# Kernel tuning notes

Measured on AMD Instinct MI355X. Metric: run time of the kernel, lower is better.

## Reference

```python
import jax, jax.numpy as jnp
import numpy as np

E = 64  # embedding_size
N_NODES = 100000
N_FACTS = 100000  # ground facts per relation
ARITY_GROUPS = {1: 2, 2: 3, 3: 2, 4: 1}  # arity -> number of relations with that arity


def mish(x):
    return x * jnp.tanh(jax.nn.softplus(x))


def _group_messages(node_embeddings, idx, wi, bi, wo, bo, arity):
    # idx: [G, F*arity] flat node indices for G relations of this arity
    G, L = idx.shape
    x = node_embeddings[idx]                      # [G, F*arity, E] gather
    x = x.reshape(G, L // arity, arity * E)       # [G, F, arity*E]
    h = mish(jnp.einsum('gfi,goi->gfo', x, wi) + bi[:, None, :])
    y = jnp.einsum('gfi,goi->gfo', h, wo) + bo[:, None, :]
    msgs = (x + y).reshape(-1, E)                 # residual, back to [G*F*arity, E]
    return msgs, idx.reshape(-1)


def setup_inputs():
    key = jax.random.key(0)
    ks = jax.random.split(key, 16)
    inp = {"node_embeddings": jax.random.normal(ks[0], (N_NODES, E), jnp.float32)}
    k = 1
    for a, G in ARITY_GROUPS.items():
        d = a * E
        inp[f"idx_a{a}"] = jax.random.randint(ks[k], (G, N_FACTS * a), 0, N_NODES); k += 1
        inp[f"wi_a{a}"] = jax.random.normal(ks[k], (G, d, d), jnp.float32) / np.sqrt(d).astype(np.float32); k += 1
        inp[f"bi_a{a}"] = jnp.zeros((G, d), jnp.float32)
        inp[f"wo_a{a}"] = jax.random.normal(ks[k], (G, d, d), jnp.float32) / np.sqrt(d).astype(np.float32); k += 1
        inp[f"bo_a{a}"] = jnp.zeros((G, d), jnp.float32)
    return inp


def reference(node_embeddings,
              idx_a1, wi_a1, bi_a1, wo_a1, bo_a1,
              idx_a2, wi_a2, bi_a2, wo_a2, bo_a2,
              idx_a3, wi_a3, bi_a3, wo_a3, bo_a3,
              idx_a4, wi_a4, bi_a4, wo_a4, bo_a4):
    groups = [
        (idx_a1, wi_a1, bi_a1, wo_a1, bo_a1, 1),
        (idx_a2, wi_a2, bi_a2, wo_a2, bo_a2, 2),
        (idx_a3, wi_a3, bi_a3, wo_a3, bo_a3, 3),
        (idx_a4, wi_a4, bi_a4, wo_a4, bo_a4, 4),
    ]
    msgs_list, idx_list = [], []
    for idx, wi, bi, wo, bo, a in groups:  # fixed small loop over arity groups
        m, i = _group_messages(node_embeddings, idx, wi, bi, wo, bo, a)
        msgs_list.append(m)
        idx_list.append(i)
    output_messages = jnp.concatenate(msgs_list, axis=0)   # [sum G*F*a, E]
    output_indices = jnp.concatenate(idx_list, axis=0)
    return output_messages, output_indices
```

## Files before the change

kernel.cpp:

```cpp
#include <hip/hip_runtime.h>
#include <hip/hip_bf16.h>

#define NF 100000
#define TM 64
#define NB 1563

typedef __attribute__((ext_vector_type(8))) short bf16x8;
typedef __attribute__((ext_vector_type(4))) short bf16x4;
typedef __attribute__((ext_vector_type(4))) float f32x4;

__device__ __forceinline__ short bfs(float x) {
    union { __hip_bfloat16 h; short s; } u;
    u.h = __float2bfloat16(x);
    return u.s;
}

__device__ __forceinline__ float b2f(short s) {
    union { float f; unsigned u; } u;
    u.u = ((unsigned)(unsigned short)s) << 16;
    return u.f;
}

__device__ __forceinline__ bf16x8 cvt8(const float4 a, const float4 b) {
    bf16x8 r;
    r[0] = bfs(a.x); r[1] = bfs(a.y); r[2] = bfs(a.z); r[3] = bfs(a.w);
    r[4] = bfs(b.x); r[5] = bfs(b.y); r[6] = bfs(b.z); r[7] = bfs(b.w);
    return r;
}

__device__ __forceinline__ float mish_f(float v) {
    float t = __expf(v);
    float p = t * (t + 2.0f);
    float r = v * p * __builtin_amdgcn_rcpf(p + 2.0f);
    return (v > 20.0f) ? v : r;
}

struct CvtA {
    const float* src[8];
    long pre[9];
    int  Dv[8];
    const float* emb;
    long embElems;
};

__global__ __launch_bounds__(256)
void cvt_all(CvtA a, __hip_bfloat16* __restrict__ dst) {
    long e = ((long)blockIdx.x * 256 + threadIdx.x) * 8;
    if (e < a.embElems) {
        const float4* s = (const float4*)(a.emb + e);
        *(bf16x8*)(dst + e) = cvt8(s[0], s[1]);
        return;
    }
    long we = e - a.embElems;
    if (we >= a.pre[8]) return;
    int j = 0;
    #pragma unroll
    for (int q = 0; q < 8; q++) if (we >= a.pre[q + 1]) j = q + 1;
    long le = we - a.pre[j];
    const int D = a.Dv[j];
    int g = (int)(le / ((long)D * D));
    int rem = (int)(le - (long)g * D * D);
    int n = rem / D;
    int k = rem - n * D;
    const float4* s = (const float4*)(a.src[j] + le);
    long off = a.embElems + a.pre[j] + (long)g * D * D + (long)(k >> 5) * 32 * D + n * 32 + (k & 31);
    *(bf16x8*)(dst + off) = cvt8(s[0], s[1]);
}

template<int D, int A, int MINW>
__global__ __launch_bounds__(256, MINW)
void msg3_kernel(const __hip_bfloat16* __restrict__ emb,
                 const int* __restrict__ idx,
                 const __hip_bfloat16* __restrict__ wi, const float* __restrict__ bi,
                 const __hip_bfloat16* __restrict__ wo, const float* __restrict__ bo,
                 float* __restrict__ out_msgs, float* __restrict__ out_idx)
{
    constexpr int DP = D + 8;
    constexpr int CT = D / 64;
    constexpr int KS = D / 32;
    constexpr int RC = D / 8;
    constexpr int CH = (TM * RC) / 256;
    constexpr bool FULLW = (D <= 128);
    __shared__ __hip_bfloat16 buf[TM][DP];

    const int g    = blockIdx.y;
    const int f0   = blockIdx.x * TM;
    const int tid  = threadIdx.x;
    const int lane = tid & 63;
    const int w    = tid >> 6;
    const long gFA = (long)g * NF * A;
    const int valid = min(TM, NF - f0);
    const int* idx_g = idx + gFA + (long)f0 * A;

    const int ar = lane & 15;
    const int kg = lane >> 4;
    const int c0 = w * (D / 4);
    const long wlane = (long)g * D * D + (long)(c0 + ar) * 32 + kg * 8;

    {
        int nodes[CH];
        #pragma unroll
        for (int j = 0; j < CH; j++) {
            int c = tid + j * 256;
            int r = c / RC;
            nodes[j] = (r < valid) ? idx_g[r * A + ((c % RC) >> 3)] : idx_g[0];
        }
        bf16x8 v[CH];
        #pragma unroll
        for (int j = 0; j < CH; j++) {
            int c = tid + j * 256;
            v[j] = *(const bf16x8*)(emb + (long)nodes[j] * 64 + (((c % RC) * 8) & 63));
        }
        #pragma unroll
        for (int j = 0; j < CH; j++) {
            int c = tid + j * 256;
            *(bf16x8*)(&buf[c / RC][(c % RC) * 8]) = v[j];
        }
        if (tid < valid * A)
            __builtin_nontemporal_store((float)idx_g[tid], &out_idx[gFA + (long)f0 * A + tid]);
    }

    f32x4 acc[4][CT];
    #pragma unroll
    for (int rt = 0; rt < 4; rt++)
        #pragma unroll
        for (int ct = 0; ct < CT; ct++) acc[rt][ct] = (f32x4)0.0f;

    if constexpr (FULLW) {
        bf16x8 wia[KS][CT];
        #pragma unroll
        for (int ks = 0; ks < KS; ks++)
            #pragma unroll
            for (int ct = 0; ct < CT; ct++)
                wia[ks][ct] = *(const bf16x8*)(wi + wlane + (long)ks * 32 * D + ct * 512);

        __syncthreads();

        #pragma unroll
        for (int ks = 0; ks < KS; ks++) {
            const int kk = ks * 32;
            bf16x8 xb[4];
            #pragma unroll
            for (int rt = 0; rt < 4; rt++) xb[rt] = *(const bf16x8*)(&buf[rt * 16 + ar][kk + kg * 8]);
            #pragma unroll
            for (int ct = 0; ct < CT; ct++)
                #pragma unroll
                for (int rt = 0; rt < 4; rt++)
                    acc[rt][ct] = __builtin_amdgcn_mfma_f32_16x16x32_bf16(wia[ks][ct], xb[rt], acc[rt][ct], 0, 0, 0);
        }

        bf16x8 woa[KS][CT];
        #pragma unroll
        for (int ks = 0; ks < KS; ks++)
            #pragma unroll
            for (int ct = 0; ct < CT; ct++)
                woa[ks][ct] = *(const bf16x8*)(wo + wlane + (long)ks * 32 * D + ct * 512);

        bf16x4 res[4][CT];
        #pragma unroll
        for (int ct = 0; ct < CT; ct++) {
            const int cb = c0 + ct * 16 + kg * 4;
            #pragma unroll
            for (int rt = 0; rt < 4; rt++)
                res[rt][ct] = *(const bf16x4*)(&buf[rt * 16 + ar][cb]);
        }
        __syncthreads();

        #pragma unroll
        for (int ct = 0; ct < CT; ct++) {
            const int cb = c0 + ct * 16 + kg * 4;
            const float4 bi4 = *(const float4*)(bi + g * D + cb);
            #pragma unroll
            for (int rt = 0; rt < 4; rt++) {
                bf16x4 hv;
                hv[0] = bfs(mish_f(acc[rt][ct][0] + bi4.x));
                hv[1] = bfs(mish_f(acc[rt][ct][1] + bi4.y));
                hv[2] = bfs(mish_f(acc[rt][ct][2] + bi4.z));
                hv[3] = bfs(mish_f(acc[rt][ct][3] + bi4.w));
                *(bf16x4*)(&buf[rt * 16 + ar][cb]) = hv;
            }
        }
        __syncthreads();

        #pragma unroll
        for (int rt = 0; rt < 4; rt++)
            #pragma unroll
            for (int ct = 0; ct < CT; ct++) acc[rt][ct] = (f32x4)0.0f;

        #pragma unroll
        for (int ks = 0; ks < KS; ks++) {
            const int kk = ks * 32;
            bf16x8 hb[4];
            #pragma unroll
            for (int rt = 0; rt < 4; rt++) hb[rt] = *(const bf16x8*)(&buf[rt * 16 + ar][kk + kg * 8]);
            #pragma unroll
            for (int ct = 0; ct < CT; ct++)
                #pragma unroll
                for (int rt = 0; rt < 4; rt++)
                    acc[rt][ct] = __builtin_amdgcn_mfma_f32_16x16x32_bf16(woa[ks][ct], hb[rt], acc[rt][ct], 0, 0, 0);
        }

        float* ob = out_msgs + (gFA + (long)f0 * A) * 64;
        #pragma unroll
        for (int ct = 0; ct < CT; ct++) {
            const int cb = c0 + ct * 16 + kg * 4;
            const float4 bo4 = *(const float4*)(bo + g * D + cb);
            #pragma unroll
            for (int rt = 0; rt < 4; rt++) {
                const int r = rt * 16 + ar;
                f32x4 o;
                o[0] = acc[rt][ct][0] + bo4.x + b2f(res[rt][ct][0]);
                o[1] = acc[rt][ct][1] + bo4.y + b2f(res[rt][ct][1]);
                o[2] = acc[rt][ct][2] + bo4.z + b2f(res[rt][ct][2]);
                o[3] = acc[rt][ct][3] + bo4.w + b2f(res[rt][ct][3]);
                if (r < valid)
                    __builtin_nontemporal_store(o, (f32x4*)(ob + (long)r * D + cb));
            }
        }
    } else {
        bf16x8 wcur[CT];
        #pragma unroll
        for (int ct = 0; ct < CT; ct++)
            wcur[ct] = *(const bf16x8*)(wi + wlane + ct * 512);

        __syncthreads();

        #pragma unroll
        for (int ks = 0; ks < KS; ks++) {
            bf16x8 wnx[CT];
            if (ks + 1 < KS)
                #pragma unroll
                for (int ct = 0; ct < CT; ct++)
                    wnx[ct] = *(const bf16x8*)(wi + wlane + (long)(ks + 1) * 32 * D + ct * 512);
            const int kk = ks * 32;
            bf16x8 xb[4];
            #pragma unroll
            for (int rt = 0; rt < 4; rt++) xb[rt] = *(const bf16x8*)(&buf[rt * 16 + ar][kk + kg * 8]);
            #pragma unroll
            for (int ct = 0; ct < CT; ct++)
                #pragma unroll
                for (int rt = 0; rt < 4; rt++)
                    acc[rt][ct] = __builtin_amdgcn_mfma_f32_16x16x32_bf16(wcur[ct], xb[rt], acc[rt][ct], 0, 0, 0);
            if (ks + 1 < KS)
                #pragma unroll
                for (int ct = 0; ct < CT; ct++) wcur[ct] = wnx[ct];
        }

        #pragma unroll
        for (int ct = 0; ct < CT; ct++)
            wcur[ct] = *(const bf16x8*)(wo + wlane + ct * 512);

        bf16x4 res[4][CT];
        #pragma unroll
        for (int ct = 0; ct < CT; ct++) {
            const int cb = c0 + ct * 16 + kg * 4;
            #pragma unroll
            for (int rt = 0; rt < 4; rt++)
                res[rt][ct] = *(const bf16x4*)(&buf[rt * 16 + ar][cb]);
        }
        __syncthreads();

        #pragma unroll
        for (int ct = 0; ct < CT; ct++) {
            const int cb = c0 + ct * 16 + kg * 4;
            const float4 bi4 = *(const float4*)(bi + g * D + cb);
            #pragma unroll
            for (int rt = 0; rt < 4; rt++) {
                bf16x4 hv;
                hv[0] = bfs(mish_f(acc[rt][ct][0] + bi4.x));
                hv[1] = bfs(mish_f(acc[rt][ct][1] + bi4.y));
                hv[2] = bfs(mish_f(acc[rt][ct][2] + bi4.z));
                hv[3] = bfs(mish_f(acc[rt][ct][3] + bi4.w));
                *(bf16x4*)(&buf[rt * 16 + ar][cb]) = hv;
            }
        }
        __syncthreads();

        #pragma unroll
        for (int rt = 0; rt < 4; rt++)
            #pragma unroll
            for (int ct = 0; ct < CT; ct++) acc[rt][ct] = (f32x4)0.0f;

        #pragma unroll
        for (int ks = 0; ks < KS; ks++) {
            bf16x8 wnx[CT];
            if (ks + 1 < KS)
                #pragma unroll
                for (int ct = 0; ct < CT; ct++)
                    wnx[ct] = *(const bf16x8*)(wo + wlane + (long)(ks + 1) * 32 * D + ct * 512);
            const int kk = ks * 32;
            bf16x8 hb[4];
            #pragma unroll
            for (int rt = 0; rt < 4; rt++) hb[rt] = *(const bf16x8*)(&buf[rt * 16 + ar][kk + kg * 8]);
            #pragma unroll
            for (int ct = 0; ct < CT; ct++)
                #pragma unroll
                for (int rt = 0; rt < 4; rt++)
                    acc[rt][ct] = __builtin_amdgcn_mfma_f32_16x16x32_bf16(wcur[ct], hb[rt], acc[rt][ct], 0, 0, 0);
            if (ks + 1 < KS)
                #pragma unroll
                for (int ct = 0; ct < CT; ct++) wcur[ct] = wnx[ct];
        }

        float* ob = out_msgs + (gFA + (long)f0 * A) * 64;
        #pragma unroll
        for (int ct = 0; ct < CT; ct++) {
            const int cb = c0 + ct * 16 + kg * 4;
            const float4 bo4 = *(const float4*)(bo + g * D + cb);
            #pragma unroll
            for (int rt = 0; rt < 4; rt++) {
                const int r = rt * 16 + ar;
                f32x4 o;
                o[0] = acc[rt][ct][0] + bo4.x + b2f(res[rt][ct][0]);
                o[1] = acc[rt][ct][1] + bo4.y + b2f(res[rt][ct][1]);
                o[2] = acc[rt][ct][2] + bo4.z + b2f(res[rt][ct][2]);
                o[3] = acc[rt][ct][3] + bo4.w + b2f(res[rt][ct][3]);
                if (r < valid)
                    __builtin_nontemporal_store(o, (f32x4*)(ob + (long)r * D + cb));
            }
        }
    }
}

template<int D, int A, int MINW>
__global__ __launch_bounds__(256, MINW)
void msg_kernel(const float* __restrict__ embv,
                const int* __restrict__ idx,
                const float* __restrict__ wiv, const float* __restrict__ bi,
                const float* __restrict__ wov, const float* __restrict__ bo,
                float* __restrict__ out_msgs, float* __restrict__ out_idx)
{
    constexpr int DP = D + 8;
    constexpr int CT = D / 64;
    constexpr int KS = D / 32;
    constexpr int RC = D / 8;
    __shared__ __hip_bfloat16 buf[TM][DP];

    const int g    = blockIdx.y;
    const int f0   = blockIdx.x * TM;
    const int tid  = threadIdx.x;
    const int lane = tid & 63;
    const int w    = tid >> 6;
    const long gFA = (long)g * NF * A;
    const int valid = min(TM, NF - f0);

    {
        const int* idx_g = idx + gFA + (long)f0 * A;
        #pragma unroll
        for (int c = tid; c < TM * RC; c += 256) {
            int r = c / RC;
            int i = (c - r * RC) * 8;
            bf16x8 v = (bf16x8)0;
            if (r < valid) {
                int node = idx_g[r * A + (i >> 6)];
                const float4* s = (const float4*)(embv + (long)node * 64 + (i & 63));
                v = cvt8(s[0], s[1]);
            }
            *(bf16x8*)(&buf[r][i]) = v;
        }
        if (tid < valid * A) out_idx[gFA + (long)f0 * A + tid] = (float)idx_g[tid];
    }
    __syncthreads();

    const int ar = lane & 15;
    const int kg = lane >> 4;
    const int c0 = w * (D / 4);
    const long wbase = (long)g * D * D;

    f32x4 acc[4][CT];
    #pragma unroll
    for (int rt = 0; rt < 4; rt++)
        #pragma unroll
        for (int ct = 0; ct < CT; ct++) acc[rt][ct] = (f32x4)0.0f;

    #pragma unroll
    for (int ks = 0; ks < KS; ks++) {
        const int kk = ks * 32;
        bf16x8 xb[4];
        #pragma unroll
        for (int rt = 0; rt < 4; rt++) xb[rt] = *(const bf16x8*)(&buf[rt * 16 + ar][kk + kg * 8]);
        #pragma unroll
        for (int ct = 0; ct < CT; ct++) {
            const float4* bp = (const float4*)(wiv + wbase + (long)(c0 + ct * 16 + ar) * D + kk + kg * 8);
            bf16x8 wf = cvt8(bp[0], bp[1]);
            #pragma unroll
            for (int rt = 0; rt < 4; rt++)
                acc[rt][ct] = __builtin_amdgcn_mfma_f32_16x16x32_bf16(wf, xb[rt], acc[rt][ct], 0, 0, 0);
        }
    }

    bf16x4 res[4][CT];
    #pragma unroll
    for (int ct = 0; ct < CT; ct++) {
        const int cb = c0 + ct * 16 + kg * 4;
        #pragma unroll
        for (int rt = 0; rt < 4; rt++)
            res[rt][ct] = *(const bf16x4*)(&buf[rt * 16 + ar][cb]);
    }
    __syncthreads();

    #pragma unroll
    for (int ct = 0; ct < CT; ct++) {
        const int cb = c0 + ct * 16 + kg * 4;
        const float4 bi4 = *(const float4*)(bi + g * D + cb);
        #pragma unroll
        for (int rt = 0; rt < 4; rt++) {
            bf16x4 hv;
            hv[0] = bfs(mish_f(acc[rt][ct][0] + bi4.x));
            hv[1] = bfs(mish_f(acc[rt][ct][1] + bi4.y));
            hv[2] = bfs(mish_f(acc[rt][ct][2] + bi4.z));
            hv[3] = bfs(mish_f(acc[rt][ct][3] + bi4.w));
            *(bf16x4*)(&buf[rt * 16 + ar][cb]) = hv;
        }
    }
    __syncthreads();

    #pragma unroll
    for (int rt = 0; rt < 4; rt++)
        #pragma unroll
        for (int ct = 0; ct < CT; ct++) acc[rt][ct] = (f32x4)0.0f;

    #pragma unroll
    for (int ks = 0; ks < KS; ks++) {
        const int kk = ks * 32;
        bf16x8 hb[4];
        #pragma unroll
        for (int rt = 0; rt < 4; rt++) hb[rt] = *(const bf16x8*)(&buf[rt * 16 + ar][kk + kg * 8]);
        #pragma unroll
        for (int ct = 0; ct < CT; ct++) {
            const float4* bp = (const float4*)(wov + wbase + (long)(c0 + ct * 16 + ar) * D + kk + kg * 8);
            bf16x8 wf = cvt8(bp[0], bp[1]);
            #pragma unroll
            for (int rt = 0; rt < 4; rt++)
                acc[rt][ct] = __builtin_amdgcn_mfma_f32_16x16x32_bf16(wf, hb[rt], acc[rt][ct], 0, 0, 0);
        }
    }

    {
        float* ob = out_msgs + (gFA + (long)f0 * A) * 64;
        #pragma unroll
        for (int ct = 0; ct < CT; ct++) {
            const int cb = c0 + ct * 16 + kg * 4;
            const float4 bo4 = *(const float4*)(bo + g * D + cb);
            #pragma unroll
            for (int rt = 0; rt < 4; rt++) {
                const int r = rt * 16 + ar;
                float4 o;
                o.x = acc[rt][ct][0] + bo4.x + b2f(res[rt][ct][0]);
                o.y = acc[rt][ct][1] + bo4.y + b2f(res[rt][ct][1]);
                o.z = acc[rt][ct][2] + bo4.z + b2f(res[rt][ct][2]);
                o.w = acc[rt][ct][3] + bo4.w + b2f(res[rt][ct][3]);
                if (r < valid) *(float4*)(ob + (long)r * D + cb) = o;
            }
        }
    }
}

extern "C" void kernel_launch(void* const* d_in, const int* in_sizes, int n_in,
                              void* d_out, int out_size, void* d_ws, size_t ws_size,
                              hipStream_t stream) {
    const float* emb_f = (const float*)d_in[0];
    const int Gs[4] = {2, 3, 2, 1};
    const int Ds[4] = {64, 128, 192, 256};

    const int*   idx_a[4];
    const float *wi_f[4], *bi_f[4], *wo_f[4], *bo_f[4];
    for (int k = 0; k < 4; k++) {
        idx_a[k] = (const int*)d_in[1 + 5 * k];
        wi_f[k]  = (const float*)d_in[2 + 5 * k];
        bi_f[k]  = (const float*)d_in[3 + 5 * k];
        wo_f[k]  = (const float*)d_in[4 + 5 * k];
        bo_f[k]  = (const float*)d_in[5 + 5 * k];
    }

    float* out = (float*)d_out;
    const long MSG_ELEMS = 115200000L;
    const long rowOff[4] = {0, 200000, 800000, 1400000};
    float* om[4]; float* oi[4];
    for (int k = 0; k < 4; k++) {
        om[k] = out + rowOff[k] * 64;
        oi[k] = out + MSG_ELEMS + rowOff[k];
    }

    const long EMB_ELEMS = 6400000L;
    long wPre[9]; wPre[0] = 0;
    int  wD[8];
    for (int k = 0; k < 4; k++) {
        long we = (long)Gs[k] * Ds[k] * Ds[k];
        wPre[2 * k + 1] = wPre[2 * k] + we;
        wPre[2 * k + 2] = wPre[2 * k + 1] + we;
        wD[2 * k] = Ds[k]; wD[2 * k + 1] = Ds[k];
    }
    const long NEED = (EMB_ELEMS + wPre[8]) * 2;

    if (ws_size >= (size_t)NEED) {
        __hip_bfloat16* emb_b = (__hip_bfloat16*)d_ws;
        __hip_bfloat16* w_b   = emb_b + EMB_ELEMS;

        CvtA ca;
        for (int k = 0; k < 4; k++) { ca.src[2 * k] = wi_f[k]; ca.src[2 * k + 1] = wo_f[k]; }
        for (int j = 0; j < 9; j++) ca.pre[j] = wPre[j];
        for (int j = 0; j < 8; j++) ca.Dv[j] = wD[j];
        ca.emb = emb_f;
        ca.embElems = EMB_ELEMS;
        long totChunks = (EMB_ELEMS + wPre[8]) / 8;
        cvt_all<<<dim3((totChunks + 255) / 256), dim3(256), 0, stream>>>(ca, emb_b);

        const __hip_bfloat16 *wi_b[4], *wo_b[4];
        for (int k = 0; k < 4; k++) { wi_b[k] = w_b + wPre[2 * k]; wo_b[k] = w_b + wPre[2 * k + 1]; }

        msg3_kernel<64, 1, 4><<<dim3(NB, 2), 256, 0, stream>>>(
            emb_b, idx_a[0], wi_b[0], bi_f[0], wo_b[0], bo_f[0], om[0], oi[0]);
        msg3_kernel<128, 2, 4><<<dim3(NB, 3), 256, 0, stream>>>(
            emb_b, idx_a[1], wi_b[1], bi_f[1], wo_b[1], bo_f[1], om[1], oi[1]);
        msg3_kernel<192, 3, 4><<<dim3(NB, 2), 256, 0, stream>>>(
            emb_b, idx_a[2], wi_b[2], bi_f[2], wo_b[2], bo_f[2], om[2], oi[2]);
        msg3_kernel<256, 4, 3><<<dim3(NB, 1), 256, 0, stream>>>(
            emb_b, idx_a[3], wi_b[3], bi_f[3], wo_b[3], bo_f[3], om[3], oi[3]);
    } else {
        msg_kernel<64, 1, 4><<<dim3(NB, 2), 256, 0, stream>>>(
            emb_f, idx_a[0], wi_f[0], bi_f[0], wo_f[0], bo_f[0], om[0], oi[0]);
        msg_kernel<128, 2, 4><<<dim3(NB, 3), 256, 0, stream>>>(
            emb_f, idx_a[1], wi_f[1], bi_f[1], wo_f[1], bo_f[1], om[1], oi[1]);
        msg_kernel<192, 3, 4><<<dim3(NB, 2), 256, 0, stream>>>(
            emb_f, idx_a[2], wi_f[2], bi_f[2], wo_f[2], bo_f[2], om[2], oi[2]);
        msg_kernel<256, 4, 3><<<dim3(NB, 1), 256, 0, stream>>>(
            emb_f, idx_a[3], wi_f[3], bi_f[3], wo_f[3], bo_f[3], om[3], oi[3]);
    }
}
```

Before: 207.3 us.

## Fuse four arity kernels into one launch with per-block dispatch

Replaces the four per-arity kernel launches with a single fused kernel that picks the arity group from the block index, heaviest groups first, sharing one maximal LDS buffer. The intent is to remove launch gaps and tail effects between the per-arity kernels and let the groups overlap on the device. For D=256 a new mode streams weights from global memory per k-step without register double-buffering, and the large-D residual is re-gathered from the bf16 embeddings at store time instead of held in registers. This cuts register pressure but adds extra gather loads, and the shared LDS size and the single launch-bounds setting of 4 may reduce occupancy for the small-D blocks.

```diff
diff --git a/kernel.cpp b/kernel.cpp
--- a/kernel.cpp
+++ b/kernel.cpp
@@ -67,24 +67,22 @@
     *(bf16x8*)(dst + off) = cvt8(s[0], s[1]);
 }
 
-template<int D, int A, int MINW>
-__global__ __launch_bounds__(256, MINW)
-void msg3_kernel(const __hip_bfloat16* __restrict__ emb,
-                 const int* __restrict__ idx,
-                 const __hip_bfloat16* __restrict__ wi, const float* __restrict__ bi,
-                 const __hip_bfloat16* __restrict__ wo, const float* __restrict__ bo,
-                 float* __restrict__ out_msgs, float* __restrict__ out_idx)
+template<int D, int A, int WMODE>
+__device__ __forceinline__ void body(
+    int fb, int g,
+    const __hip_bfloat16* __restrict__ emb, const int* __restrict__ idx,
+    const __hip_bfloat16* __restrict__ wi, const float* __restrict__ bi,
+    const __hip_bfloat16* __restrict__ wo, const float* __restrict__ bo,
+    float* __restrict__ out_msgs, float* __restrict__ out_idx,
+    __hip_bfloat16* __restrict__ buf)
 {
     constexpr int DP = D + 8;
     constexpr int CT = D / 64;
     constexpr int KS = D / 32;
     constexpr int RC = D / 8;
     constexpr int CH = (TM * RC) / 256;
-    constexpr bool FULLW = (D <= 128);
-    __shared__ __hip_bfloat16 buf[TM][DP];
-
-    const int g    = blockIdx.y;
-    const int f0   = blockIdx.x * TM;
+
+    const int f0   = fb * TM;
     const int tid  = threadIdx.x;
     const int lane = tid & 63;
     const int w    = tid >> 6;
@@ -114,7 +112,7 @@
         #pragma unroll
         for (int j = 0; j < CH; j++) {
             int c = tid + j * 256;
-            *(bf16x8*)(&buf[c / RC][(c % RC) * 8]) = v[j];
+            *(bf16x8*)(buf + (c / RC) * DP + (c % RC) * 8) = v[j];
         }
         if (tid < valid * A)
             __builtin_nontemporal_store((float)idx_g[tid], &out_idx[gFA + (long)f0 * A + tid]);
@@ -126,7 +124,7 @@
         #pragma unroll
         for (int ct = 0; ct < CT; ct++) acc[rt][ct] = (f32x4)0.0f;
 
-    if constexpr (FULLW) {
+    if constexpr (WMODE == 0) {
         bf16x8 wia[KS][CT];
         #pragma unroll
         for (int ks = 0; ks < KS; ks++)
@@ -141,7 +139,8 @@
             const int kk = ks * 32;
             bf16x8 xb[4];
             #pragma unroll
-            for (int rt = 0; rt < 4; rt++) xb[rt] = *(const bf16x8*)(&buf[rt * 16 + ar][kk + kg * 8]);
+            for (int rt = 0; rt < 4; rt++)
+                xb[rt] = *(const bf16x8*)(buf + (rt * 16 + ar) * DP + kk + kg * 8);
             #pragma unroll
             for (int ct = 0; ct < CT; ct++)
                 #pragma unroll
@@ -162,7 +161,7 @@
             const int cb = c0 + ct * 16 + kg * 4;
             #pragma unroll
             for (int rt = 0; rt < 4; rt++)
-                res[rt][ct] = *(const bf16x4*)(&buf[rt * 16 + ar][cb]);
+                res[rt][ct] = *(const bf16x4*)(buf + (rt * 16 + ar) * DP + cb);
         }
         __syncthreads();
 
@@ -177,7 +176,7 @@
                 hv[1] = bfs(mish_f(acc[rt][ct][1] + bi4.y));
                 hv[2] = bfs(mish_f(acc[rt][ct][2] + bi4.z));
                 hv[3] = bfs(mish_f(acc[rt][ct][3] + bi4.w));
-                *(bf16x4*)(&buf[rt * 16 + ar][cb]) = hv;
+                *(bf16x4*)(buf + (rt * 16 + ar) * DP + cb) = hv;
             }
         }
         __syncthreads();
@@ -192,7 +191,8 @@
             const int kk = ks * 32;
             bf16x8 hb[4];
             #pragma unroll
-            for (int rt = 0; rt < 4; rt++) hb[rt] = *(const bf16x8*)(&buf[rt * 16 + ar][kk + kg * 8]);
+            for (int rt = 0; rt < 4; rt++)
+                hb[rt] = *(const bf16x8*)(buf + (rt * 16 + ar) * DP + kk + kg * 8);
             #pragma unroll
             for (int ct = 0; ct < CT; ct++)
                 #pragma unroll
@@ -219,45 +219,45 @@
         }
     } else {
         bf16x8 wcur[CT];
-        #pragma unroll
-        for (int ct = 0; ct < CT; ct++)
-            wcur[ct] = *(const bf16x8*)(wi + wlane + ct * 512);
-
+        if constexpr (WMODE == 1) {
+            #pragma unroll
+            for (int ct = 0; ct < CT; ct++)
+                wcur[ct] = *(const bf16x8*)(wi + wlane + ct * 512);
+        }
         __syncthreads();
 
         #pragma unroll
         for (int ks = 0; ks < KS; ks++) {
-            bf16x8 wnx[CT];
-            if (ks + 1 < KS)
+            const int kk = ks * 32;
+            bf16x8 xb[4];
+            #pragma unroll
+            for (int rt = 0; rt < 4; rt++)
+                xb[rt] = *(const bf16x8*)(buf + (rt * 16 + ar) * DP + kk + kg * 8);
+            if constexpr (WMODE == 1) {
+                bf16x8 wnx[CT];
+                if (ks + 1 < KS)
+                    #pragma unroll
+                    for (int ct = 0; ct < CT; ct++)
+                        wnx[ct] = *(const bf16x8*)(wi + wlane + (long)(ks + 1) * 32 * D + ct * 512);
                 #pragma unroll
                 for (int ct = 0; ct < CT; ct++)
-                    wnx[ct] = *(const bf16x8*)(wi + wlane + (long)(ks + 1) * 32 * D + ct * 512);
-            const int kk = ks * 32;
-            bf16x8 xb[4];
-            #pragma unroll
-            for (int rt = 0; rt < 4; rt++) xb[rt] = *(const bf16x8*)(&buf[rt * 16 + ar][kk + kg * 8]);
-            #pragma unroll
-            for (int ct = 0; ct < CT; ct++)
+                    #pragma unroll
+                    for (int rt = 0; rt < 4; rt++)
+                        acc[rt][ct] = __builtin_amdgcn_mfma_f32_16x16x32_bf16(wcur[ct], xb[rt], acc[rt][ct], 0, 0, 0);
+                if (ks + 1 < KS)
+                    #pragma unroll
+                    for (int ct = 0; ct < CT; ct++) wcur[ct] = wnx[ct];
+            } else {
                 #pragma unroll
-                for (int rt = 0; rt < 4; rt++)
-                    acc[rt][ct] = __builtin_amdgcn_mfma_f32_16x16x32_bf16(wcur[ct], xb[rt], acc[rt][ct], 0, 0, 0);
-            if (ks + 1 < KS)
-                #pragma unroll
-                for (int ct = 0; ct < CT; ct++) wcur[ct] = wnx[ct];
-        }
-
-        #pragma unroll
-        for (int ct = 0; ct < CT; ct++)
-            wcur[ct] = *(const bf16x8*)(wo + wlane + ct * 512);
-
-        bf16x4 res[4][CT];
-        #pragma unroll
-        for (int ct = 0; ct < CT; ct++) {
-            const int cb = c0 + ct * 16 + kg * 4;
-            #pragma unroll
-            for (int rt = 0; rt < 4; rt++)
-                res[rt][ct] = *(const bf16x4*)(&buf[rt * 16 + ar][cb]);
-        }
+                for (int ct = 0; ct < CT; ct++) {
+                    bf16x8 wf = *(const bf16x8*)(wi + wlane + (long)ks * 32 * D + ct * 512);
+                    #pragma unroll
+                    for (int rt = 0; rt < 4; rt++)
+                        acc[rt][ct] = __builtin_amdgcn_mfma_f32_16x16x32_bf16(wf, xb[rt], acc[rt][ct], 0, 0, 0);
+                }
+            }
+        }
+
         __syncthreads();
 
         #pragma unroll
@@ -271,7 +271,7 @@
                 hv[1] = bfs(mish_f(acc[rt][ct][1] + bi4.y));
                 hv[2] = bfs(mish_f(acc[rt][ct][2] + bi4.z));
                 hv[3] = bfs(mish_f(acc[rt][ct][3] + bi4.w));
-                *(bf16x4*)(&buf[rt * 16 + ar][cb]) = hv;
+                *(bf16x4*)(buf + (rt * 16 + ar) * DP + cb) = hv;
             }
         }
         __syncthreads();
@@ -281,44 +281,90 @@
             #pragma unroll
             for (int ct = 0; ct < CT; ct++) acc[rt][ct] = (f32x4)0.0f;
 
+        if constexpr (WMODE == 1) {
+            #pragma unroll
+            for (int ct = 0; ct < CT; ct++)
+                wcur[ct] = *(const bf16x8*)(wo + wlane + ct * 512);
+        }
+
         #pragma unroll
         for (int ks = 0; ks < KS; ks++) {
-            bf16x8 wnx[CT];
-            if (ks + 1 < KS)
+            const int kk = ks * 32;
+            bf16x8 hb[4];
+            #pragma unroll
+            for (int rt = 0; rt < 4; rt++)
+                hb[rt] = *(const bf16x8*)(buf + (rt * 16 + ar) * DP + kk + kg * 8);
+            if constexpr (WMODE == 1) {
+                bf16x8 wnx[CT];
+                if (ks + 1 < KS)
+                    #pragma unroll
+                    for (int ct = 0; ct < CT; ct++)
+                        wnx[ct] = *(const bf16x8*)(wo + wlane + (long)(ks + 1) * 32 * D + ct * 512);
                 #pragma unroll
                 for (int ct = 0; ct < CT; ct++)
-                    wnx[ct] = *(const bf16x8*)(wo + wlane + (long)(ks + 1) * 32 * D + ct * 512);
-            const int kk = ks * 32;
-            bf16x8 hb[4];
-            #pragma unroll
-            for (int rt = 0; rt < 4; rt++) hb[rt] = *(const bf16x8*)(&buf[rt * 16 + ar][kk + kg * 8]);
-            #pragma unroll
-            for (int ct = 0; ct < CT; ct++)
+                    #pragma unroll
+                    for (int rt = 0; rt < 4; rt++)
+                        acc[rt][ct] = __builtin_amdgcn_mfma_f32_16x16x32_bf16(wcur[ct], hb[rt], acc[rt][ct], 0, 0, 0);
+                if (ks + 1 < KS)
+                    #pragma unroll
+                    for (int ct = 0; ct < CT; ct++) wcur[ct] = wnx[ct];
+            } else {
                 #pragma unroll
-                for (int rt = 0; rt < 4; rt++)
-                    acc[rt][ct] = __builtin_amdgcn_mfma_f32_16x16x32_bf16(wcur[ct], hb[rt], acc[rt][ct], 0, 0, 0);
-            if (ks + 1 < KS)
-                #pragma unroll
-                for (int ct = 0; ct < CT; ct++) wcur[ct] = wnx[ct];
+                for (int ct = 0; ct < CT; ct++) {
+                    bf16x8 wf = *(const bf16x8*)(wo + wlane + (long)ks * 32 * D + ct * 512);
+                    #pragma unroll
+                    for (int rt = 0; rt < 4; rt++)
+                        acc[rt][ct] = __builtin_amdgcn_mfma_f32_16x16x32_bf16(wf, hb[rt], acc[rt][ct], 0, 0, 0);
+                }
+            }
         }
 
         float* ob = out_msgs + (gFA + (long)f0 * A) * 64;
         #pragma unroll
         for (int ct = 0; ct < CT; ct++) {
             const int cb = c0 + ct * 16 + kg * 4;
+            const int sres = (c0 + ct * 16) >> 6;
             const float4 bo4 = *(const float4*)(bo + g * D + cb);
             #pragma unroll
             for (int rt = 0; rt < 4; rt++) {
                 const int r = rt * 16 + ar;
+                int node = idx_g[min(r, valid - 1) * A + sres];
+                bf16x4 xv = *(const bf16x4*)(emb + (long)node * 64 + (cb & 63));
                 f32x4 o;
-                o[0] = acc[rt][ct][0] + bo4.x + b2f(res[rt][ct][0]);
-                o[1] = acc[rt][ct][1] + bo4.y + b2f(res[rt][ct][1]);
-                o[2] = acc[rt][ct][2] + bo4.z + b2f(res[rt][ct][2]);
-                o[3] = acc[rt][ct][3] + bo4.w + b2f(res[rt][ct][3]);
+                o[0] = acc[rt][ct][0] + bo4.x + b2f(xv[0]);
+                o[1] = acc[rt][ct][1] + bo4.y + b2f(xv[1]);
+                o[2] = acc[rt][ct][2] + bo4.z + b2f(xv[2]);
+                o[3] = acc[rt][ct][3] + bo4.w + b2f(xv[3]);
                 if (r < valid)
                     __builtin_nontemporal_store(o, (f32x4*)(ob + (long)r * D + cb));
             }
         }
+    }
+}
+
+struct KArgs {
+    const __hip_bfloat16* emb;
+    const int* idx[4];
+    const __hip_bfloat16* wi[4]; const float* bi[4];
+    const __hip_bfloat16* wo[4]; const float* bo[4];
+    float* om[4]; float* oi[4];
+};
+
+__global__ __launch_bounds__(256, 4)
+void fused_kernel(KArgs a) {
+    __shared__ __hip_bfloat16 buf[TM * 264];
+    const int b = blockIdx.x;
+    if (b < NB) {
+        body<256, 4, 2>(b, 0, a.emb, a.idx[3], a.wi[3], a.bi[3], a.wo[3], a.bo[3], a.om[3], a.oi[3], buf);
+    } else if (b < NB * 3) {
+        int r = b - NB;
+        body<192, 3, 1>(r % NB, r / NB, a.emb, a.idx[2], a.wi[2], a.bi[2], a.wo[2], a.bo[2], a.om[2], a.oi[2], buf);
+    } else if (b < NB * 6) {
+        int r = b - NB * 3;
+        body<128, 2, 0>(r % NB, r / NB, a.emb, a.idx[1], a.wi[1], a.bi[1], a.wo[1], a.bo[1], a.om[1], a.oi[1], buf);
+    } else {
+        int r = b - NB * 6;
+        body<64, 1, 0>(r % NB, r / NB, a.emb, a.idx[0], a.wi[0], a.bi[0], a.wo[0], a.bo[0], a.om[0], a.oi[0], buf);
     }
 }
 
@@ -506,17 +552,18 @@
         long totChunks = (EMB_ELEMS + wPre[8]) / 8;
         cvt_all<<<dim3((totChunks + 255) / 256), dim3(256), 0, stream>>>(ca, emb_b);
 
-        const __hip_bfloat16 *wi_b[4], *wo_b[4];
-        for (int k = 0; k < 4; k++) { wi_b[k] = w_b + wPre[2 * k]; wo_b[k] = w_b + wPre[2 * k + 1]; }
-
-        msg3_kernel<64, 1, 4><<<dim3(NB, 2), 256, 0, stream>>>(
-            emb_b, idx_a[0], wi_b[0], bi_f[0], wo_b[0], bo_f[0], om[0], oi[0]);
-        msg3_kernel<128, 2, 4><<<dim3(NB, 3), 256, 0, stream>>>(
-            emb_b, idx_a[1], wi_b[1], bi_f[1], wo_b[1], bo_f[1], om[1], oi[1]);
-        msg3_kernel<192, 3, 4><<<dim3(NB, 2), 256, 0, stream>>>(
-            emb_b, idx_a[2], wi_b[2], bi_f[2], wo_b[2], bo_f[2], om[2], oi[2]);
-        msg3_kernel<256, 4, 3><<<dim3(NB, 1), 256, 0, stream>>>(
-            emb_b, idx_a[3], wi_b[3], bi_f[3], wo_b[3], bo_f[3], om[3], oi[3]);
+        KArgs a;
+        a.emb = emb_b;
+        for (int k = 0; k < 4; k++) {
+            a.idx[k] = idx_a[k];
+            a.wi[k] = w_b + wPre[2 * k];
+            a.wo[k] = w_b + wPre[2 * k + 1];
+            a.bi[k] = bi_f[k];
+            a.bo[k] = bo_f[k];
+            a.om[k] = om[k];
+            a.oi[k] = oi[k];
+        }
+        fused_kernel<<<dim3(NB * 8), dim3(256), 0, stream>>>(a);
     } else {
         msg_kernel<64, 1, 4><<<dim3(NB, 2), 256, 0, stream>>>(
             emb_f, idx_a[0], wi_f[0], bi_f[0], wo_f[0], bo_f[0], om[0], oi[0]);
```

Result: faster. 200.3 us (-3.4%).
